# Kernel tuning notes

Measured on AMD Instinct MI355X. Metric: run time of the kernel, lower is better.

Reference implementation:

```python
import jax, jax.numpy as jnp
import numpy as np

DIM = 1024
N_HEADS = 16
HEAD_DIM = DIM // N_HEADS
SCALE = HEAD_DIM ** (-0.5)


def setup_inputs() -> dict:
    key = jax.random.key(0)
    ks = jax.random.split(key, 5)
    B, N = 2, 2048
    x = jax.random.normal(ks[0], (B, N, DIM), dtype=jnp.float32)
    # torch nn.Linear weight layout: (out_features, in_features)
    qkv_w = jax.random.normal(ks[1], (3 * DIM, DIM), dtype=jnp.float32) * 0.02
    qkv_b = jax.random.normal(ks[2], (3 * DIM,), dtype=jnp.float32) * 0.02
    proj_w = jax.random.normal(ks[3], (DIM, DIM), dtype=jnp.float32) * 0.02
    proj_b = jax.random.normal(ks[4], (DIM,), dtype=jnp.float32) * 0.02
    return {"x": x, "qkv_w": qkv_w, "qkv_b": qkv_b, "proj_w": proj_w, "proj_b": proj_b}


def reference(x, qkv_w, qkv_b, proj_w, proj_b):
    B, N, C = x.shape
    # QKV projection: (B,N,C) -> (B,N,3C)
    qkv = jnp.einsum('bnc,oc->bno', x, qkv_w) + qkv_b
    # (B,N,3,H,Dh) -> (3,B,H,N,Dh)
    qkv = qkv.reshape(B, N, 3, N_HEADS, HEAD_DIM).transpose(2, 0, 3, 1, 4)
    q, k, v = qkv[0], qkv[1], qkv[2]
    attn = jnp.einsum('bhqd,bhkd->bhqk', q, k) * SCALE
    attn = jax.nn.softmax(attn, axis=-1)
    out = jnp.einsum('bhqk,bhkd->bhqd', attn, v)
    out = out.transpose(0, 2, 1, 3).reshape(B, N, C)  # concat heads
    out = jnp.einsum('bnc,oc->bno', out, proj_w) + proj_b
    return out
```

## Files before the change

kernel.cpp:

```cpp
#include <hip/hip_runtime.h>

#define DIM 1024
#define NHEADS 16
#define HD 64
#define NSEQ 2048
#define MROWS 4096
#define QKV_LD 3072

typedef __attribute__((ext_vector_type(8))) short short8;
typedef __attribute__((ext_vector_type(4))) float f32x4;

typedef __attribute__((address_space(1))) void gvoid_t;
typedef __attribute__((address_space(3))) void lvoid_t;

#if __has_builtin(__builtin_amdgcn_exp2f)
#define EXP2(x) __builtin_amdgcn_exp2f(x)
#else
#define EXP2(x) exp2f(x)
#endif

#define EXP_SCALE 0.18033688011112042f

__device__ __forceinline__ unsigned short f2bf(float f) {
  unsigned int u = __builtin_bit_cast(unsigned int, f);
  u += 0x7FFFu + ((u >> 16) & 1u);
  return (unsigned short)(u >> 16);
}

__device__ __forceinline__ void gl_lds16(const void* g, void* l) {
  __builtin_amdgcn_global_load_lds((gvoid_t*)g, (lvoid_t*)l, 16, 0, 0);
}

__global__ __launch_bounds__(256) void cast_bf16_3(
    const float* __restrict__ x, const float* __restrict__ wq,
    const float* __restrict__ wp,
    unsigned short* __restrict__ xb, unsigned short* __restrict__ wqb,
    unsigned short* __restrict__ wpb)
{
  int g = blockIdx.x * 256 + threadIdx.x;
  const float* src;
  unsigned short* dst;
  if (g < 1048576)            { src = x  + (size_t)g * 4;              dst = xb  + (size_t)g * 4; }
  else if (g < 1048576 + 786432) { int t = g - 1048576; src = wq + (size_t)t * 4; dst = wqb + (size_t)t * 4; }
  else                        { int t = g - 1048576 - 786432; src = wp + (size_t)t * 4; dst = wpb + (size_t)t * 4; }
  float4 v = *(const float4*)src;
  ushort4 o;
  o.x = f2bf(v.x); o.y = f2bf(v.y); o.z = f2bf(v.z); o.w = f2bf(v.w);
  *(ushort4*)dst = o;
}

__global__ __launch_bounds__(256) void gemm_nt(
    const unsigned short* __restrict__ A,
    const unsigned short* __restrict__ Bw,
    const float* __restrict__ bias,
    int K, int mode,
    unsigned short* __restrict__ oq,
    unsigned short* __restrict__ ovt,
    float* __restrict__ of)
{
  __shared__ unsigned short As[128 * 32];
  __shared__ unsigned short Bs[128 * 32];

  const int tid  = threadIdx.x;
  const int wave = tid >> 6, lane = tid & 63;
  const int quad = lane >> 4, l15 = lane & 15;
  const int mblk = blockIdx.x * 128;
  const int nblk = blockIdx.y * 128;
  const int wrow = (wave >> 1) * 64, wcol = (wave & 1) * 64;

  f32x4 acc[4][4] = {};

  const int sr = lane >> 2;
  const int sq = (lane & 3) ^ (sr & 3);
  const unsigned short* aBase = A  + (size_t)(mblk + wave * 32 + sr) * K + sq * 8;
  const unsigned short* bBase = Bw + (size_t)(nblk + wave * 32 + sr) * K + sq * 8;

  for (int k0 = 0; k0 < K; k0 += 32) {
    __syncthreads();
    gl_lds16(aBase + k0,          As + (wave * 32) * 32);
    gl_lds16(aBase + 16 * K + k0, As + (wave * 32 + 16) * 32);
    gl_lds16(bBase + k0,          Bs + (wave * 32) * 32);
    gl_lds16(bBase + 16 * K + k0, Bs + (wave * 32 + 16) * 32);
    __syncthreads();

    short8 af[4], bf8[4];
#pragma unroll
    for (int mt = 0; mt < 4; ++mt) {
      int row = wrow + mt * 16 + l15;
      af[mt] = *(const short8*)(As + row * 32 + ((quad ^ (row & 3)) * 8));
    }
#pragma unroll
    for (int nt = 0; nt < 4; ++nt) {
      int row = wcol + nt * 16 + l15;
      bf8[nt] = *(const short8*)(Bs + row * 32 + ((quad ^ (row & 3)) * 8));
    }
#pragma unroll
    for (int mt = 0; mt < 4; ++mt)
#pragma unroll
      for (int nt = 0; nt < 4; ++nt)
        acc[mt][nt] = __builtin_amdgcn_mfma_f32_16x16x32_bf16(af[mt], bf8[nt], acc[mt][nt], 0, 0, 0);
  }

  float bv[4];
#pragma unroll
  for (int nt = 0; nt < 4; ++nt) bv[nt] = bias[nblk + wcol + nt * 16 + l15];

  if (mode == 0) {
#pragma unroll
    for (int mt = 0; mt < 4; ++mt) {
      int row0 = mblk + wrow + mt * 16 + quad * 4;
#pragma unroll
      for (int nt = 0; nt < 4; ++nt) {
        int col = nblk + wcol + nt * 16 + l15;
#pragma unroll
        for (int r = 0; r < 4; ++r)
          of[(size_t)(row0 + r) * DIM + col] = acc[mt][nt][r] + bv[nt];
      }
    }
  } else if (nblk < 2048) {
#pragma unroll
    for (int mt = 0; mt < 4; ++mt) {
      int row0 = mblk + wrow + mt * 16 + quad * 4;
#pragma unroll
      for (int nt = 0; nt < 4; ++nt) {
        int col = nblk + wcol + nt * 16 + l15;
#pragma unroll
        for (int r = 0; r < 4; ++r)
          oq[(size_t)(row0 + r) * QKV_LD + col] = f2bf(acc[mt][nt][r] + bv[nt]);
      }
    }
  } else {
#pragma unroll
    for (int mt = 0; mt < 4; ++mt) {
      int row0 = mblk + wrow + mt * 16 + quad * 4;
      int n0 = row0 & (NSEQ - 1);
      int bb = row0 >> 11;
#pragma unroll
      for (int nt = 0; nt < 4; ++nt) {
        int colr = (nblk - 2048) + wcol + nt * 16 + l15;
        int bh = bb * NHEADS + (colr >> 6);
        int d  = colr & 63;
        ushort4 pk;
        pk.x = f2bf(acc[mt][nt][0] + bv[nt]);
        pk.y = f2bf(acc[mt][nt][1] + bv[nt]);
        pk.z = f2bf(acc[mt][nt][2] + bv[nt]);
        pk.w = f2bf(acc[mt][nt][3] + bv[nt]);
        *(ushort4*)(ovt + ((size_t)bh * HD + d) * NSEQ + n0) = pk;
      }
    }
  }
}

__global__ __launch_bounds__(256) void gemm_nt64(
    const unsigned short* __restrict__ A,
    const unsigned short* __restrict__ Bw,
    const float* __restrict__ bias,
    int K,
    float* __restrict__ of)
{
  __shared__ unsigned short As[64 * 32];
  __shared__ unsigned short Bs[128 * 32];

  const int tid  = threadIdx.x;
  const int wave = tid >> 6, lane = tid & 63;
  const int quad = lane >> 4, l15 = lane & 15;
  const int mblk = blockIdx.x * 64;
  const int nblk = blockIdx.y * 128;
  const int wrow = (wave >> 1) * 32, wcol = (wave & 1) * 64;

  f32x4 acc[2][4] = {};

  const int sr = lane >> 2;
  const int sq = (lane & 3) ^ (sr & 3);
  const unsigned short* aBase = A  + (size_t)(mblk + wave * 16 + sr) * K + sq * 8;
  const unsigned short* bBase = Bw + (size_t)(nblk + wave * 32 + sr) * K + sq * 8;

  for (int k0 = 0; k0 < K; k0 += 32) {
    __syncthreads();
    gl_lds16(aBase + k0,          As + (wave * 16) * 32);
    gl_lds16(bBase + k0,          Bs + (wave * 32) * 32);
    gl_lds16(bBase + 16 * K + k0, Bs + (wave * 32 + 16) * 32);
    __syncthreads();

    short8 af[2], bf8[4];
#pragma unroll
    for (int mt = 0; mt < 2; ++mt) {
      int row = wrow + mt * 16 + l15;
      af[mt] = *(const short8*)(As + row * 32 + ((quad ^ (row & 3)) * 8));
    }
#pragma unroll
    for (int nt = 0; nt < 4; ++nt) {
      int row = wcol + nt * 16 + l15;
      bf8[nt] = *(const short8*)(Bs + row * 32 + ((quad ^ (row & 3)) * 8));
    }
#pragma unroll
    for (int mt = 0; mt < 2; ++mt)
#pragma unroll
      for (int nt = 0; nt < 4; ++nt)
        acc[mt][nt] = __builtin_amdgcn_mfma_f32_16x16x32_bf16(af[mt], bf8[nt], acc[mt][nt], 0, 0, 0);
  }

  float bv[4];
#pragma unroll
  for (int nt = 0; nt < 4; ++nt) bv[nt] = bias[nblk + wcol + nt * 16 + l15];

#pragma unroll
  for (int mt = 0; mt < 2; ++mt) {
    int row0 = mblk + wrow + mt * 16 + quad * 4;
#pragma unroll
    for (int nt = 0; nt < 4; ++nt) {
      int col = nblk + wcol + nt * 16 + l15;
#pragma unroll
      for (int r = 0; r < 4; ++r)
        of[(size_t)(row0 + r) * DIM + col] = acc[mt][nt][r] + bv[nt];
    }
  }
}

__global__ __launch_bounds__(256, 4) void attn_fused(
    const unsigned short* __restrict__ qkv,
    const unsigned short* __restrict__ vt,
    unsigned short* __restrict__ aout)
{
  __shared__ unsigned short Ks[64 * 64];
  __shared__ unsigned short Vs[64 * 64];
  __shared__ unsigned short Ps[4][16 * 64];

  const int tid  = threadIdx.x;
  const int wave = tid >> 6, lane = tid & 63;
  const int quad = lane >> 4, l15 = lane & 15;
  const int bh = blockIdx.x, b = bh >> 4, h = bh & 15;
  const int q0 = blockIdx.y * 64;

  const size_t qkvB = (size_t)b * NSEQ * QKV_LD;

  short8 qf[2];
#pragma unroll
  for (int ks = 0; ks < 2; ++ks)
    qf[ks] = *(const short8*)(qkv + qkvB +
        (size_t)(q0 + wave * 16 + l15) * QKV_LD + h * HD + ks * 32 + quad * 8);

  f32x4 oacc[4] = {};
  float lsum[4] = {};

  const int sr8 = lane >> 3;
  const int sp8 = lane & 7;

  const unsigned short* kBase = qkv + qkvB + DIM + h * HD;
  const unsigned short* vBase = vt + (size_t)bh * HD * NSEQ;

  for (int kk = 0; kk < NSEQ; kk += 64) {
    __syncthreads();
#pragma unroll
    for (int i = 0; i < 2; ++i) {
      int r  = wave * 16 + i * 8 + sr8;
      int qc = sp8 ^ (r & 7);
      gl_lds16(kBase + (size_t)(kk + r) * QKV_LD + qc * 8, Ks + (wave * 16 + i * 8) * 64);
      gl_lds16(vBase + (size_t)r * NSEQ + kk + qc * 8,     Vs + (wave * 16 + i * 8) * 64);
    }
    __syncthreads();

    short8 kf[4][2];
#pragma unroll
    for (int kt = 0; kt < 4; ++kt)
#pragma unroll
      for (int ks = 0; ks < 2; ++ks) {
        int row = kt * 16 + l15;
        kf[kt][ks] = *(const short8*)(Ks + row * 64 + (((ks * 4 + quad) ^ (row & 7)) * 8));
      }

    f32x4 sacc[4] = {};
#pragma unroll
    for (int kt = 0; kt < 4; ++kt) {
      sacc[kt] = __builtin_amdgcn_mfma_f32_16x16x32_bf16(qf[0], kf[kt][0], sacc[kt], 0, 0, 0);
      sacc[kt] = __builtin_amdgcn_mfma_f32_16x16x32_bf16(qf[1], kf[kt][1], sacc[kt], 0, 0, 0);
    }

#pragma unroll
    for (int kt = 0; kt < 4; ++kt)
#pragma unroll
      for (int r = 0; r < 4; ++r) {
        float p = EXP2(sacc[kt][r] * EXP_SCALE);
        lsum[r] += p;
        int rowl = quad * 4 + r;
        int key  = kt * 16 + l15;
        Ps[wave][rowl * 64 + (((key >> 3) ^ (rowl & 7)) * 8) + (key & 7)] = f2bf(p);
      }

    __asm__ volatile("s_waitcnt lgkmcnt(0)" ::: "memory");

    short8 pf[2], vf[4][2];
#pragma unroll
    for (int ks = 0; ks < 2; ++ks) {
      int rowl = l15;
      pf[ks] = *(const short8*)(&Ps[wave][rowl * 64 + (((ks * 4 + quad) ^ (rowl & 7)) * 8)]);
    }
#pragma unroll
    for (int dt = 0; dt < 4; ++dt)
#pragma unroll
      for (int ks = 0; ks < 2; ++ks) {
        int row = dt * 16 + l15;
        vf[dt][ks] = *(const short8*)(Vs + row * 64 + (((ks * 4 + quad) ^ (row & 7)) * 8));
      }
#pragma unroll
    for (int dt = 0; dt < 4; ++dt) {
      oacc[dt] = __builtin_amdgcn_mfma_f32_16x16x32_bf16(pf[0], vf[dt][0], oacc[dt], 0, 0, 0);
      oacc[dt] = __builtin_amdgcn_mfma_f32_16x16x32_bf16(pf[1], vf[dt][1], oacc[dt], 0, 0, 0);
    }
  }

#pragma unroll
  for (int r = 0; r < 4; ++r) {
    float s = lsum[r];
    s += __shfl_xor(s, 1);
    s += __shfl_xor(s, 2);
    s += __shfl_xor(s, 4);
    s += __shfl_xor(s, 8);
    float inv = 1.0f / s;
    int n = q0 + wave * 16 + quad * 4 + r;
#pragma unroll
    for (int dt = 0; dt < 4; ++dt)
      aout[(size_t)(b * NSEQ + n) * DIM + h * HD + dt * 16 + l15] =
          f2bf(oacc[dt][r] * inv);
  }
}

extern "C" void kernel_launch(void* const* d_in, const int* in_sizes, int n_in,
                              void* d_out, int out_size, void* d_ws, size_t ws_size,
                              hipStream_t stream) {
  (void)in_sizes; (void)n_in; (void)out_size; (void)ws_size;
  const float* x      = (const float*)d_in[0];
  const float* qkv_w  = (const float*)d_in[1];
  const float* qkv_b  = (const float*)d_in[2];
  const float* proj_w = (const float*)d_in[3];
  const float* proj_b = (const float*)d_in[4];
  float* out = (float*)d_out;

  char* ws = (char*)d_ws;
  unsigned short* xb   = (unsigned short*)(ws);
  unsigned short* wqb  = (unsigned short*)(ws + ( 8u << 20));
  unsigned short* wpb  = (unsigned short*)(ws + (14u << 20));
  unsigned short* qkv  = (unsigned short*)(ws + (16u << 20));
  unsigned short* vtw  = (unsigned short*)(ws + (40u << 20));
  unsigned short* attn = (unsigned short*)(ws + (48u << 20));

  cast_bf16_3<<<8192, 256, 0, stream>>>(x, qkv_w, proj_w, xb, wqb, wpb);
  gemm_nt<<<dim3(32, 24), 256, 0, stream>>>(xb, wqb, qkv_b, DIM, 1, qkv, vtw, nullptr);
  attn_fused<<<dim3(32, 32), 256, 0, stream>>>(qkv, vtw, attn);
  gemm_nt64<<<dim3(64, 8), 256, 0, stream>>>(attn, wpb, proj_b, DIM, out);
}
```

Measured before the change: 201.8 us.

## Keep softmax probabilities in registers by transposing S and using 16x16x16 MFMA for PV

The attention kernel computes S transposed (K as the A operand), so each lane's accumulator holds four consecutive keys for one query. These probabilities are packed straight into bf16 operands for a 16x16x16 MFMA against V, which removes the per-wave LDS scratch buffer, its stores and loads, and the wait. The row-sum reduction and output store are also simplified into packed 8-byte writes. In exchange the PV product uses twice as many smaller MFMAs, and bf16 rounding becomes round-half-up instead of round-to-nearest-even.

Result: faster. 197.8 us (-2.0%).

```diff
diff --git a/kernel.cpp b/kernel.cpp
--- a/kernel.cpp
+++ b/kernel.cpp
@@ -8,6 +8,7 @@
 #define QKV_LD 3072
 
 typedef __attribute__((ext_vector_type(8))) short short8;
+typedef __attribute__((ext_vector_type(4))) short short4v;
 typedef __attribute__((ext_vector_type(4))) float f32x4;
 
 typedef __attribute__((address_space(1))) void gvoid_t;
@@ -17,6 +18,18 @@
 #define EXP2(x) __builtin_amdgcn_exp2f(x)
 #else
 #define EXP2(x) exp2f(x)
+#endif
+
+#if __has_builtin(__builtin_amdgcn_mfma_f32_16x16x16_bf16)
+#define MFMA16(a, b, c) __builtin_amdgcn_mfma_f32_16x16x16_bf16(a, b, c, 0, 0, 0)
+#elif __has_builtin(__builtin_amdgcn_mfma_f32_16x16x16bf16_1k)
+#define MFMA16(a, b, c) __builtin_amdgcn_mfma_f32_16x16x16bf16_1k(a, b, c, 0, 0, 0)
+#else
+static __device__ __forceinline__ f32x4 mfma16_asm(short4v a, short4v b, f32x4 c) {
+  __asm__("v_mfma_f32_16x16x16_bf16 %0, %1, %2, %0" : "+v"(c) : "v"(a), "v"(b));
+  return c;
+}
+#define MFMA16(a, b, c) mfma16_asm(a, b, c)
 #endif
 
 #define EXP_SCALE 0.18033688011112042f
@@ -224,14 +237,12 @@
 {
   __shared__ unsigned short Ks[64 * 64];
   __shared__ unsigned short Vs[64 * 64];
-  __shared__ unsigned short Ps[4][16 * 64];
 
   const int tid  = threadIdx.x;
   const int wave = tid >> 6, lane = tid & 63;
   const int quad = lane >> 4, l15 = lane & 15;
   const int bh = blockIdx.x, b = bh >> 4, h = bh & 15;
   const int q0 = blockIdx.y * 64;
-
   const size_t qkvB = (size_t)b * NSEQ * QKV_LD;
 
   short8 qf[2];
@@ -241,7 +252,7 @@
         (size_t)(q0 + wave * 16 + l15) * QKV_LD + h * HD + ks * 32 + quad * 8);
 
   f32x4 oacc[4] = {};
-  float lsum[4] = {};
+  float lsum = 0.f;
 
   const int sr8 = lane >> 3;
   const int sp8 = lane & 7;
@@ -272,56 +283,60 @@
     f32x4 sacc[4] = {};
 #pragma unroll
     for (int kt = 0; kt < 4; ++kt) {
-      sacc[kt] = __builtin_amdgcn_mfma_f32_16x16x32_bf16(qf[0], kf[kt][0], sacc[kt], 0, 0, 0);
-      sacc[kt] = __builtin_amdgcn_mfma_f32_16x16x32_bf16(qf[1], kf[kt][1], sacc[kt], 0, 0, 0);
-    }
-
-#pragma unroll
-    for (int kt = 0; kt < 4; ++kt)
-#pragma unroll
-      for (int r = 0; r < 4; ++r) {
-        float p = EXP2(sacc[kt][r] * EXP_SCALE);
-        lsum[r] += p;
-        int rowl = quad * 4 + r;
-        int key  = kt * 16 + l15;
-        Ps[wave][rowl * 64 + (((key >> 3) ^ (rowl & 7)) * 8) + (key & 7)] = f2bf(p);
-      }
-
-    __asm__ volatile("s_waitcnt lgkmcnt(0)" ::: "memory");
-
-    short8 pf[2], vf[4][2];
-#pragma unroll
-    for (int ks = 0; ks < 2; ++ks) {
-      int rowl = l15;
-      pf[ks] = *(const short8*)(&Ps[wave][rowl * 64 + (((ks * 4 + quad) ^ (rowl & 7)) * 8)]);
-    }
-#pragma unroll
-    for (int dt = 0; dt < 4; ++dt)
-#pragma unroll
-      for (int ks = 0; ks < 2; ++ks) {
-        int row = dt * 16 + l15;
-        vf[dt][ks] = *(const short8*)(Vs + row * 64 + (((ks * 4 + quad) ^ (row & 7)) * 8));
-      }
+      sacc[kt] = __builtin_amdgcn_mfma_f32_16x16x32_bf16(kf[kt][0], qf[0], sacc[kt], 0, 0, 0);
+      sacc[kt] = __builtin_amdgcn_mfma_f32_16x16x32_bf16(kf[kt][1], qf[1], sacc[kt], 0, 0, 0);
+    }
+
+    short4v vf[4][4];
 #pragma unroll
     for (int dt = 0; dt < 4; ++dt) {
-      oacc[dt] = __builtin_amdgcn_mfma_f32_16x16x32_bf16(pf[0], vf[dt][0], oacc[dt], 0, 0, 0);
-      oacc[dt] = __builtin_amdgcn_mfma_f32_16x16x32_bf16(pf[1], vf[dt][1], oacc[dt], 0, 0, 0);
-    }
-  }
-
-#pragma unroll
-  for (int r = 0; r < 4; ++r) {
-    float s = lsum[r];
-    s += __shfl_xor(s, 1);
-    s += __shfl_xor(s, 2);
-    s += __shfl_xor(s, 4);
-    s += __shfl_xor(s, 8);
-    float inv = 1.0f / s;
-    int n = q0 + wave * 16 + quad * 4 + r;
-#pragma unroll
-    for (int dt = 0; dt < 4; ++dt)
-      aout[(size_t)(b * NSEQ + n) * DIM + h * HD + dt * 16 + l15] =
-          f2bf(oacc[dt][r] * inv);
+      int row = dt * 16 + l15;
+      int rw  = row & 7;
+      const unsigned short* vb = Vs + row * 64 + (quad & 1) * 4;
+#pragma unroll
+      for (int kt = 0; kt < 4; ++kt) {
+        int phys = (2 * kt + (quad >> 1)) ^ rw;
+        vf[dt][kt] = *(const short4v*)(vb + phys * 8);
+      }
+    }
+
+#pragma unroll
+    for (int kt = 0; kt < 4; ++kt) {
+      float p0 = EXP2(sacc[kt][0] * EXP_SCALE);
+      float p1 = EXP2(sacc[kt][1] * EXP_SCALE);
+      float p2 = EXP2(sacc[kt][2] * EXP_SCALE);
+      float p3 = EXP2(sacc[kt][3] * EXP_SCALE);
+      lsum += (p0 + p1) + (p2 + p3);
+      unsigned r0 = __builtin_bit_cast(unsigned, p0) + 0x8000u;
+      unsigned r1 = __builtin_bit_cast(unsigned, p1) + 0x8000u;
+      unsigned r2 = __builtin_bit_cast(unsigned, p2) + 0x8000u;
+      unsigned r3 = __builtin_bit_cast(unsigned, p3) + 0x8000u;
+      uint2 pd;
+      pd.x = __builtin_amdgcn_perm(r1, r0, 0x07060302u);
+      pd.y = __builtin_amdgcn_perm(r3, r2, 0x07060302u);
+      short4v pf = __builtin_bit_cast(short4v, pd);
+#pragma unroll
+      for (int dt = 0; dt < 4; ++dt)
+        oacc[dt] = MFMA16(vf[dt][kt], pf, oacc[dt]);
+    }
+  }
+
+  lsum += __shfl_xor(lsum, 16);
+  lsum += __shfl_xor(lsum, 32);
+  float inv = 1.0f / lsum;
+
+  const int qrow = q0 + wave * 16 + l15;
+  const size_t outBase = (size_t)(b * NSEQ + qrow) * DIM + h * HD;
+#pragma unroll
+  for (int dt = 0; dt < 4; ++dt) {
+    unsigned a0 = __builtin_bit_cast(unsigned, oacc[dt][0] * inv) + 0x8000u;
+    unsigned a1 = __builtin_bit_cast(unsigned, oacc[dt][1] * inv) + 0x8000u;
+    unsigned a2 = __builtin_bit_cast(unsigned, oacc[dt][2] * inv) + 0x8000u;
+    unsigned a3 = __builtin_bit_cast(unsigned, oacc[dt][3] * inv) + 0x8000u;
+    uint2 st;
+    st.x = __builtin_amdgcn_perm(a1, a0, 0x07060302u);
+    st.y = __builtin_amdgcn_perm(a3, a2, 0x07060302u);
+    *(uint2*)(aout + outBase + dt * 16 + quad * 4) = st;
   }
 }
 
```
